# Kernel tuning notes

Hardware: AMD Instinct MI355X
Metric: run time of the kernel (lower is better)

The kernel has to match this reference:

```python
import jax, jax.numpy as jnp
import numpy as np
import math

B, S, D, H = 8, 1024, 512, 8
DH = D // H
SCALE_BASE = 512


def _xpos(x, downscale):
    # x: [B, H, S, DH]; xpos rotary with exponential scale (jamie-stirling RetNet impl)
    s = x.shape[-2]
    d = x.shape[-1]
    half = d // 2
    sv = (jnp.arange(0, d, 2, dtype=jnp.float32) + 0.4 * d) / (1.4 * d)      # [half]
    power = jnp.arange(s, dtype=jnp.float32) / SCALE_BASE
    scale = sv[None, :] ** power[:, None]                                     # [s, half]
    inv_freq = 1.0 / (10000.0 ** (jnp.arange(half, dtype=jnp.float32) / half))
    ang = jnp.arange(s, dtype=jnp.float32)[:, None] * inv_freq[None, :]       # [s, half]
    if downscale:
        scale = 1.0 / scale
    sin = jnp.repeat(jnp.sin(ang) * scale, 2, axis=-1)                        # [s, d]
    cos = jnp.repeat(jnp.cos(ang) * scale, 2, axis=-1)
    rot = jnp.stack((-x[..., 1::2], x[..., ::2]), axis=-1).reshape(x.shape)   # rotate_every_two
    return x * cos + rot * sin


def setup_inputs() -> dict:
    key = jax.random.key(0)
    ks = jax.random.split(key, 7)
    X = jax.random.normal(ks[0], (B, S, D), dtype=jnp.float32)
    # per-head projections stacked: torch init randn/hidden_size
    W_Q = jax.random.normal(ks[1], (H, D, DH), dtype=jnp.float32) / D
    W_K = jax.random.normal(ks[2], (H, D, DH), dtype=jnp.float32) / D
    W_V = jax.random.normal(ks[3], (H, D, DH), dtype=jnp.float32) / D
    W_G = jax.random.normal(ks[4], (D, D), dtype=jnp.float32) / D
    W_O = jax.random.normal(ks[5], (D, D), dtype=jnp.float32) / D
    gn_weight = jnp.ones((D,), dtype=jnp.float32)
    gn_bias = jnp.zeros((D,), dtype=jnp.float32)
    return {"X": X, "W_Q": W_Q, "W_K": W_K, "W_V": W_V, "W_G": W_G,
            "W_O": W_O, "gn_weight": gn_weight, "gn_bias": gn_bias}


def reference(X, W_Q, W_K, W_V, W_G, W_O, gn_weight, gn_bias):
    b, s, _ = X.shape
    # per-head decay gammas and symmetric (non-causal) decay matrix D
    gammas = 1.0 - jnp.exp(jnp.linspace(math.log(1.0 / 32), math.log(1.0 / 512), H)).astype(jnp.float32)
    n = jnp.arange(s)
    Dmat = gammas[:, None, None] ** jnp.abs(n[:, None] - n[None, :]).astype(jnp.float32)  # [H,s,s]
    Q = _xpos(jnp.einsum('bsd,hde->bhse', X, W_Q), False)
    K = _xpos(jnp.einsum('bsd,hde->bhse', X, W_K), True)
    V = jnp.einsum('bsd,hde->bhse', X, W_V)
    scores = jnp.einsum('bhse,bhte->bhst', Q, K)
    p = jax.nn.softmax(scores, axis=-1) * Dmat[None]          # decay-weighted softmax
    Y = jnp.einsum('bhst,bhte->bhse', p, V)                    # [b,H,s,DH]
    Y = jnp.moveaxis(Y, 1, 2).reshape(b, s, H * DH)            # concat heads -> [b,s,D]
    # GroupNorm(H groups) over flattened rows [b*s, D]
    Yg = Y.reshape(-1, H, DH)
    mu = Yg.mean(axis=-1, keepdims=True)
    var = Yg.var(axis=-1, keepdims=True)
    Yn = ((Yg - mu) * jax.lax.rsqrt(var + 1e-5)).reshape(-1, H * DH)
    Yn = (Yn * gn_weight + gn_bias).reshape(b, s, H * DH)
    G = X @ W_G
    swish = G * jax.nn.sigmoid(G)
    return (swish * Yn) @ W_O
```

## Files before the change

### kernel.cpp

```cpp
#include <hip/hip_runtime.h>
#include <math.h>

#define B_ 8
#define S_ 1024
#define D_ 512
#define H_ 8
#define DH_ 64
#define M_ (B_*S_)

typedef __attribute__((ext_vector_type(8))) short short8;
typedef __attribute__((ext_vector_type(4))) short s16x4;
typedef __attribute__((ext_vector_type(4))) float f32x4;

__device__ inline void tsplit(float x, short& hs, short& ls) {
  unsigned u = __float_as_uint(x);
  hs = (short)(u >> 16);
  float r = x - __uint_as_float(u & 0xFFFF0000u);
  ls = (short)(__float_as_uint(r) >> 16);
}
__device__ inline f32x4 mfma16(short8 a, short8 b, f32x4 c) {
  return __builtin_amdgcn_mfma_f32_16x16x32_bf16(a, b, c, 0, 0, 0);
}
__device__ inline void gload_lds16(const void* g, void* l) {
  __builtin_amdgcn_global_load_lds(
      (const __attribute__((address_space(1))) void*)g,
      (__attribute__((address_space(3))) void*)l, 16, 0, 0);
}

__global__ void xpos_table_kernel(float* __restrict__ tab) {
  int idx = blockIdx.x * 256 + threadIdx.x;
  int s = idx >> 5, i = idx & 31;
  float sv = (2.0f * (float)i + 0.4f * 64.0f) / (1.4f * 64.0f);
  float p = (float)s / 512.0f;
  float scale = powf(sv, p);
  float inv_freq = powf(10000.0f, -((float)i / 32.0f));
  float ang = (float)s * inv_freq;
  float sn = sinf(ang), cs = cosf(ang);
  tab[idx]          = cs * scale;
  tab[32768 + idx]  = sn * scale;
  tab[65536 + idx]  = cs / scale;
  tab[98304 + idx]  = sn / scale;
}

__global__ __launch_bounds__(256) void wprep_kernel(
    const float* __restrict__ Wq, const float* __restrict__ Wk,
    const float* __restrict__ Wv, const float* __restrict__ Wg,
    short* __restrict__ BTh, short* __restrict__ BTl, int gonly) {
  __shared__ float t[64][65];
  const int n0 = blockIdx.x * 64, k0 = blockIdx.y * 64;
  const int tid = threadIdx.x;
  const float* src;
  int ld;
  if (gonly) {
    src = Wg + (size_t)k0 * 512 + n0; ld = 512;
  } else {
    int w = n0 >> 9, nn = n0 & 511;
    if (w == 3) { src = Wg + (size_t)k0 * 512 + nn; ld = 512; }
    else {
      const float* W = (w == 0) ? Wq : ((w == 1) ? Wk : Wv);
      int h = nn >> 6;
      src = W + (size_t)h * D_ * DH_ + (size_t)k0 * 64; ld = 64;
    }
  }
#pragma unroll
  for (int i = 0; i < 4; ++i) {
    int idx = tid + i * 256;
    int kk = idx >> 4, nl4 = (idx & 15) * 4;
    float4 v = *(const float4*)(src + (size_t)kk * ld + nl4);
    t[kk][nl4] = v.x; t[kk][nl4 + 1] = v.y; t[kk][nl4 + 2] = v.z; t[kk][nl4 + 3] = v.w;
  }
  __syncthreads();
#pragma unroll
  for (int i = 0; i < 2; ++i) {
    int idx = tid + i * 256;
    int nl = idx >> 3, ck = idx & 7;
    short8 hh, ll;
#pragma unroll
    for (int j = 0; j < 8; ++j) {
      short h_, l_;
      tsplit(t[ck * 8 + j][nl], h_, l_);
      hh[j] = h_; ll[j] = l_;
    }
    size_t off = (size_t)(n0 + nl) * 512 + k0 + ck * 8;
    *(short8*)(BTh + off) = hh;
    *(short8*)(BTl + off) = ll;
  }
}

template<int AMODE, int NSUB>
__global__ __launch_bounds__(256) void gemm_mfma_kernel(
    const float* __restrict__ Af,
    const short* __restrict__ Ah, const short* __restrict__ Al,
    const short* __restrict__ BTh, const short* __restrict__ BTl,
    const float* __restrict__ tab,
    short* __restrict__ QhO, short* __restrict__ QlO,
    short* __restrict__ KhO, short* __restrict__ KlO,
    short* __restrict__ VhT, short* __restrict__ VlT,
    float* __restrict__ G, int fused) {
  constexpr int NT = NSUB * 32;
  constexpr int ASTR = (AMODE == 0) ? 40 : 32;
  __shared__ __align__(16) short AsH[128][ASTR];
  __shared__ __align__(16) short AsL[128][ASTR];
  __shared__ __align__(16) short BsH[NT][32];
  __shared__ __align__(16) short BsL[NT][32];
  const int m0 = blockIdx.x * 128, by = blockIdx.y, n0 = by * NT;
  const int tid = threadIdx.x, w = tid >> 6, lane = tid & 63;
  const int lx = lane & 15, quad = lane >> 4;
  const int wr = w >> 1, wc = w & 1;
  f32x4 acc[4][NSUB] = {};
  for (int k0 = 0; k0 < 512; k0 += 32) {
    if constexpr (AMODE == 0) {
      int r = tid >> 1, cb = (tid & 1) * 16;
      const float* ap = Af + (size_t)(m0 + r) * 512 + k0 + cb;
      short8 hh[2], ll[2];
#pragma unroll
      for (int j4 = 0; j4 < 4; ++j4) {
        float4 v = *(const float4*)(ap + j4 * 4);
        short h_, l_;
        tsplit(v.x, h_, l_); hh[j4 >> 1][(j4 & 1) * 4 + 0] = h_; ll[j4 >> 1][(j4 & 1) * 4 + 0] = l_;
        tsplit(v.y, h_, l_); hh[j4 >> 1][(j4 & 1) * 4 + 1] = h_; ll[j4 >> 1][(j4 & 1) * 4 + 1] = l_;
        tsplit(v.z, h_, l_); hh[j4 >> 1][(j4 & 1) * 4 + 2] = h_; ll[j4 >> 1][(j4 & 1) * 4 + 2] = l_;
        tsplit(v.w, h_, l_); hh[j4 >> 1][(j4 & 1) * 4 + 3] = h_; ll[j4 >> 1][(j4 & 1) * 4 + 3] = l_;
      }
      *(short8*)&AsH[r][cb]     = hh[0];
      *(short8*)&AsH[r][cb + 8] = hh[1];
      *(short8*)&AsL[r][cb]     = ll[0];
      *(short8*)&AsL[r][cb + 8] = ll[1];
    } else {
#pragma unroll
      for (int c = 0; c < 2; ++c) {
        int ch = w + c * 4;
        size_t goff = (size_t)(m0 + ch * 16 + (lane >> 2)) * 512 + k0 + (lane & 3) * 8;
        gload_lds16(Ah + goff, &AsH[ch * 16][0]);
        gload_lds16(Al + goff, &AsL[ch * 16][0]);
      }
    }
    {
      constexpr int NCH = NT / 16;
#pragma unroll
      for (int ch = 0; ch < NCH; ch += 4) {
        int c = w + ch;
        if (c < NCH) {
          size_t goff = (size_t)(n0 + c * 16 + (lane >> 2)) * 512 + k0 + (lane & 3) * 8;
          gload_lds16(BTh + goff, &BsH[c * 16][0]);
          gload_lds16(BTl + goff, &BsL[c * 16][0]);
        }
      }
    }
    __syncthreads();
    short8 fah[4], fal[4], fbh[NSUB], fbl[NSUB];
#pragma unroll
    for (int i = 0; i < 4; ++i) {
      fah[i] = *(const short8*)&AsH[wr * 64 + i * 16 + lx][quad * 8];
      fal[i] = *(const short8*)&AsL[wr * 64 + i * 16 + lx][quad * 8];
    }
#pragma unroll
    for (int i = 0; i < NSUB; ++i) {
      fbh[i] = *(const short8*)&BsH[wc * (NSUB * 16) + i * 16 + lx][quad * 8];
      fbl[i] = *(const short8*)&BsL[wc * (NSUB * 16) + i * 16 + lx][quad * 8];
    }
#pragma unroll
    for (int ms = 0; ms < 4; ++ms)
#pragma unroll
      for (int ns = 0; ns < NSUB; ++ns) {
        f32x4 a = acc[ms][ns];
        a = mfma16(fah[ms], fbh[ns], a);
        a = mfma16(fal[ms], fbh[ns], a);
        a = mfma16(fah[ms], fbl[ns], a);
        acc[ms][ns] = a;
      }
    __syncthreads();
  }
  if (fused) {
    const int w4 = by >> 2;
    const int ncb = (by & 3) * 128 + wc * 64;
    if (w4 < 2) {
      short* Ph = (w4 == 0) ? QhO : KhO;
      short* Pl = (w4 == 0) ? QlO : KlO;
      const float* ct = tab + (w4 ? 65536 : 0);
      const float* st = tab + (w4 ? 98304 : 32768);
#pragma unroll
      for (int ms = 0; ms < 4; ++ms) {
        const int m = m0 + wr * 64 + ms * 16 + quad * 4;
        const int b = m >> 10, sbase = m & 1023;
#pragma unroll
        for (int ns = 0; ns < 4; ++ns) {
          const int n = ncb + ns * 16 + lx;
          const int h = n >> 6, e = n & 63;
          const int i0 = e >> 1;
          const float sgn = (e & 1) ? 1.0f : -1.0f;
          short* ph = Ph + (((size_t)(b * 8 + h)) * 1024 + sbase) * 64 + e;
          short* pl = Pl + (((size_t)(b * 8 + h)) * 1024 + sbase) * 64 + e;
#pragma unroll
          for (int rg = 0; rg < 4; ++rg) {
            const int s = sbase + rg;
            float v = acc[ms][ns][rg];
            float vp = __shfl_xor(v, 1);
            float o = v * ct[s * 32 + i0] + sgn * vp * st[s * 32 + i0];
            short h_, l_;
            tsplit(o, h_, l_);
            ph[rg * 64] = h_;
            pl[rg * 64] = l_;
          }
        }
      }
    } else if (w4 == 2) {
#pragma unroll
      for (int ms = 0; ms < 4; ++ms) {
        const int m = m0 + wr * 64 + ms * 16 + quad * 4;
        const int b = m >> 10, s = m & 1023;
#pragma unroll
        for (int ns = 0; ns < 4; ++ns) {
          const int n = ncb + ns * 16 + lx;
          const int h = n >> 6, e = n & 63;
          s16x4 hh, ll;
#pragma unroll
          for (int rg = 0; rg < 4; ++rg) {
            short h_, l_;
            tsplit(acc[ms][ns][rg], h_, l_);
            hh[rg] = h_; ll[rg] = l_;
          }
          size_t off = (((size_t)(b * 8 + h)) * 64 + e) * 1024 + s;
          *(s16x4*)(VhT + off) = hh;
          *(s16x4*)(VlT + off) = ll;
        }
      }
    } else {
#pragma unroll
      for (int ms = 0; ms < 4; ++ms) {
        const int m = m0 + wr * 64 + ms * 16 + quad * 4;
#pragma unroll
        for (int ns = 0; ns < 4; ++ns) {
          const int n = ncb + ns * 16 + lx;
#pragma unroll
          for (int rg = 0; rg < 4; ++rg) G[(size_t)(m + rg) * 512 + n] = acc[ms][ns][rg];
        }
      }
    }
  } else {
#pragma unroll
    for (int ms = 0; ms < 4; ++ms) {
      const int m = m0 + wr * 64 + ms * 16 + quad * 4;
#pragma unroll
      for (int ns = 0; ns < NSUB; ++ns) {
        const int n = n0 + wc * (NSUB * 16) + ns * 16 + lx;
#pragma unroll
        for (int rg = 0; rg < 4; ++rg) G[(size_t)(m + rg) * 512 + n] = acc[ms][ns][rg];
      }
    }
  }
}

__global__ __launch_bounds__(256, 2) void attn_mfma_kernel(
    const short* __restrict__ Qh, const short* __restrict__ Ql,
    const short* __restrict__ Kh, const short* __restrict__ Kl,
    const short* __restrict__ VhT, const short* __restrict__ VlT,
    const float* __restrict__ Gp,
    const float* __restrict__ gnw, const float* __restrict__ gnb,
    short* __restrict__ Zh, short* __restrict__ Zl) {
  __shared__ __align__(16) short KhS[64][72];
  __shared__ __align__(16) short KlS[64][72];
  __shared__ __align__(16) short VhS[64][72];
  __shared__ __align__(16) short VlS[64][72];
  __shared__ __align__(16) short PhS[4][32][72];
  const int bh = blockIdx.x, s0 = blockIdx.y * 128;
  const int b = bh >> 3, h = bh & 7;
  const int tid = threadIdx.x;
  const int w = tid >> 6, lane = tid & 63;
  const int lx = lane & 15, quad = lane >> 4;
  const int s0w = s0 + w * 32;
  const float l0c = -3.4657359027997265f;
  const float l1c = -6.2383246250395075f;
  const float gamma = 1.0f - expf(l0c + (float)h * (l1c - l0c) / 7.0f);
  const float lg2g = log2f(gamma);
  const short* Qbh = Qh + (size_t)bh * S_ * DH_;
  const short* Qbl = Ql + (size_t)bh * S_ * DH_;
  const short* Kbh = Kh + (size_t)bh * S_ * DH_;
  const short* Kbl = Kl + (size_t)bh * S_ * DH_;
  const short* VbH = VhT + (size_t)bh * DH_ * S_;
  const short* VbL = VlT + (size_t)bh * DH_ * S_;

  float cl[4], cr[4], w4g[4], b4g[4];
#pragma unroll
  for (int ns = 0; ns < 4; ++ns) {
    cl[ns] = exp2f(lg2g * (float)(ns * 16 + lx));
    cr[ns] = exp2f(lg2g * (float)(63 - ns * 16 - lx));
    w4g[ns] = gnw[h * DH_ + ns * 16 + lx];
    b4g[ns] = gnb[h * DH_ + ns * 16 + lx];
  }

  short8 qfh[2][2], qfl[2][2];
#pragma unroll
  for (int ms = 0; ms < 2; ++ms)
#pragma unroll
    for (int kc = 0; kc < 2; ++kc) {
      size_t off = (size_t)(s0w + ms * 16 + lx) * DH_ + kc * 32 + quad * 8;
      qfh[ms][kc] = *(const short8*)(Qbh + off);
      qfl[ms][kc] = *(const short8*)(Qbl + off);
    }

  f32x4 O[2][4] = {};
  float lsum[2][4] = {};

  for (int t0 = 0; t0 < S_; t0 += 64) {
    __syncthreads();
#pragma unroll
    for (int i = 0; i < 2; ++i) {
      int slot = tid + i * 256;
      int r = slot >> 3, c8 = (slot & 7) * 8;
      *(short8*)&KhS[r][c8] = *(const short8*)(Kbh + (size_t)(t0 + r) * DH_ + c8);
      *(short8*)&KlS[r][c8] = *(const short8*)(Kbl + (size_t)(t0 + r) * DH_ + c8);
      *(short8*)&VhS[r][c8] = *(const short8*)(VbH + (size_t)r * S_ + t0 + c8);
      *(short8*)&VlS[r][c8] = *(const short8*)(VbL + (size_t)r * S_ + t0 + c8);
    }
    __syncthreads();
    f32x4 acc[2][4];
#pragma unroll
    for (int ns = 0; ns < 4; ++ns) {
      short8 kh0 = *(const short8*)&KhS[ns * 16 + lx][quad * 8];
      short8 kh1 = *(const short8*)&KhS[ns * 16 + lx][32 + quad * 8];
      short8 kl0 = *(const short8*)&KlS[ns * 16 + lx][quad * 8];
      short8 kl1 = *(const short8*)&KlS[ns * 16 + lx][32 + quad * 8];
#pragma unroll
      for (int ms = 0; ms < 2; ++ms) {
        f32x4 a = {};
        a = mfma16(qfh[ms][0], kh0, a);
        a = mfma16(qfl[ms][0], kh0, a);
        a = mfma16(qfh[ms][0], kl0, a);
        a = mfma16(qfh[ms][1], kh1, a);
        a = mfma16(qfl[ms][1], kh1, a);
        a = mfma16(qfh[ms][1], kl1, a);
        acc[ms][ns] = a;
      }
    }
    const int cse = (t0 + 63 < s0w) ? 0 : ((t0 > s0w + 31) ? 1 : 2);
#pragma unroll
    for (int ms = 0; ms < 2; ++ms)
#pragma unroll
      for (int rg = 0; rg < 4; ++rg) {
        const int rloc = ms * 16 + quad * 4 + rg;
        const int srow = s0w + rloc;
        float pe[4], p[4];
#pragma unroll
        for (int ns = 0; ns < 4; ++ns) pe[ns] = __expf(acc[ms][ns][rg]);
        lsum[ms][rg] += (pe[0] + pe[1]) + (pe[2] + pe[3]);
        if (cse == 0) {
          float rf = exp2f(lg2g * (float)(srow - t0 - 63));
#pragma unroll
          for (int ns = 0; ns < 4; ++ns) p[ns] = pe[ns] * rf * cr[ns];
        } else if (cse == 1) {
          float rf = exp2f(lg2g * (float)(t0 - srow));
#pragma unroll
          for (int ns = 0; ns < 4; ++ns) p[ns] = pe[ns] * rf * cl[ns];
        } else {
#pragma unroll
          for (int ns = 0; ns < 4; ++ns)
            p[ns] = pe[ns] * exp2f(lg2g * fabsf((float)(srow - (t0 + ns * 16 + lx))));
        }
#pragma unroll
        for (int ns = 0; ns < 4; ++ns)
          PhS[w][rloc][ns * 16 + lx] = (short)((__float_as_uint(p[ns]) + 0x8000u) >> 16);
      }
    short8 pf[2][2];
#pragma unroll
    for (int ms = 0; ms < 2; ++ms)
#pragma unroll
      for (int kc = 0; kc < 2; ++kc)
        pf[ms][kc] = *(const short8*)&PhS[w][ms * 16 + lx][kc * 32 + quad * 8];
#pragma unroll
    for (int ns = 0; ns < 4; ++ns) {
      short8 vh0 = *(const short8*)&VhS[ns * 16 + lx][quad * 8];
      short8 vh1 = *(const short8*)&VhS[ns * 16 + lx][32 + quad * 8];
      short8 vl0 = *(const short8*)&VlS[ns * 16 + lx][quad * 8];
      short8 vl1 = *(const short8*)&VlS[ns * 16 + lx][32 + quad * 8];
#pragma unroll
      for (int ms = 0; ms < 2; ++ms) {
        f32x4 o = O[ms][ns];
        o = mfma16(pf[ms][0], vh0, o);
        o = mfma16(pf[ms][0], vl0, o);
        o = mfma16(pf[ms][1], vh1, o);
        o = mfma16(pf[ms][1], vl1, o);
        O[ms][ns] = o;
      }
    }
  }
#pragma unroll
  for (int ms = 0; ms < 2; ++ms)
#pragma unroll
    for (int rg = 0; rg < 4; ++rg) {
      float s = lsum[ms][rg];
      s += __shfl_xor(s, 1);
      s += __shfl_xor(s, 2);
      s += __shfl_xor(s, 4);
      s += __shfl_xor(s, 8);
      const float inv = 1.0f / s;
      const int srow = s0w + ms * 16 + quad * 4 + rg;
      float y[4];
      float rs = 0.0f;
#pragma unroll
      for (int ns = 0; ns < 4; ++ns) { y[ns] = O[ms][ns][rg] * inv; rs += y[ns]; }
      rs += __shfl_xor(rs, 1);
      rs += __shfl_xor(rs, 2);
      rs += __shfl_xor(rs, 4);
      rs += __shfl_xor(rs, 8);
      const float mu = rs * (1.0f / 64.0f);
      float vv = 0.0f;
#pragma unroll
      for (int ns = 0; ns < 4; ++ns) { float d = y[ns] - mu; vv += d * d; }
      vv += __shfl_xor(vv, 1);
      vv += __shfl_xor(vv, 2);
      vv += __shfl_xor(vv, 4);
      vv += __shfl_xor(vv, 8);
      const float rstd = rsqrtf(vv * (1.0f / 64.0f) + 1e-5f);
      const size_t base = (size_t)(b * S_ + srow) * D_ + h * DH_;
#pragma unroll
      for (int ns = 0; ns < 4; ++ns) {
        float g = Gp[base + ns * 16 + lx];
        float sw = g / (1.0f + __expf(-g));
        float z = sw * ((y[ns] - mu) * rstd * w4g[ns] + b4g[ns]);
        short zh_, zl_;
        tsplit(z, zh_, zl_);
        Zh[base + ns * 16 + lx] = zh_;
        Zl[base + ns * 16 + lx] = zl_;
      }
    }
}

extern "C" void kernel_launch(void* const* d_in, const int* in_sizes, int n_in,
                              void* d_out, int out_size, void* d_ws, size_t ws_size,
                              hipStream_t stream) {
  const float* X   = (const float*)d_in[0];
  const float* Wq  = (const float*)d_in[1];
  const float* Wk  = (const float*)d_in[2];
  const float* Wv  = (const float*)d_in[3];
  const float* Wg  = (const float*)d_in[4];
  const float* Wo  = (const float*)d_in[5];
  const float* gnw = (const float*)d_in[6];
  const float* gnb = (const float*)d_in[7];
  float* out = (float*)d_out;
  float* ws  = (float*)d_ws;
  const size_t NB = (size_t)M_ * D_;
  float* R0 = ws;
  float* R1 = ws + NB;
  float* R2 = ws + 2 * NB;
  float* R3 = ws + 3 * NB;
  float* tab = ws + 4 * NB;
  short* BTh = (short*)R3;
  short* BTl = BTh + (size_t)2048 * 512;
  short* Qh = (short*)R0;  short* Ql = Qh + NB;
  short* Kh = (short*)R1;  short* Kl = Kh + NB;
  short* VhT = (short*)R2; short* VlT = VhT + NB;
  short* Zh = (short*)R3;  short* Zl = Zh + NB;
  short* BToh = (short*)R1;
  short* BTol = BToh + (size_t)512 * 512;

  wprep_kernel<<<dim3(32, 8), 256, 0, stream>>>(Wq, Wk, Wv, Wg, BTh, BTl, 0);
  xpos_table_kernel<<<128, 256, 0, stream>>>(tab);
  gemm_mfma_kernel<0, 4><<<dim3(64, 16), 256, 0, stream>>>(
      X, nullptr, nullptr, BTh, BTl, tab, Qh, Ql, Kh, Kl, VhT, VlT, out, 1);
  attn_mfma_kernel<<<dim3(64, 8), 256, 0, stream>>>(
      Qh, Ql, Kh, Kl, VhT, VlT, out, gnw, gnb, Zh, Zl);
  wprep_kernel<<<dim3(8, 8), 256, 0, stream>>>(nullptr, nullptr, nullptr, Wo, BToh, BTol, 1);
  gemm_mfma_kernel<1, 2><<<dim3(64, 8), 256, 0, stream>>>(
      nullptr, Zh, Zl, BToh, BTol, nullptr, nullptr, nullptr, nullptr, nullptr,
      nullptr, nullptr, out, 0);
}
```

Baseline: 227.8 us.

## Double-buffer GEMM LDS tiles with fragment-ordered operand layouts

Reworks both MFMA GEMMs into a double-buffered pipeline: the next k-tile is loaded straight into LDS while the current tile is computed, with one barrier pair per iteration. Weights and the Z intermediate are now stored pre-tiled in MFMA-fragment order, so global-to-LDS copies are contiguous and fragment reads are simple linear LDS loads. The fp32 X operand is staged raw, with an XOR swizzle to avoid bank conflicts, and split into bf16 hi/lo at fragment-load time. The aim is to hide global load latency and cut LDS conversion work, at the cost of doubled LDS footprint and hand-tuned waitcnt counts that must match the issued loads.

```diff
diff --git a/kernel.cpp b/kernel.cpp
--- a/kernel.cpp
+++ b/kernel.cpp
@@ -11,6 +11,7 @@
 typedef __attribute__((ext_vector_type(8))) short short8;
 typedef __attribute__((ext_vector_type(4))) short s16x4;
 typedef __attribute__((ext_vector_type(4))) float f32x4;
+typedef __attribute__((ext_vector_type(4))) unsigned int u32x4;
 
 __device__ inline void tsplit(float x, short& hs, short& ls) {
   unsigned u = __float_as_uint(x);
@@ -18,6 +19,25 @@
   float r = x - __uint_as_float(u & 0xFFFF0000u);
   ls = (short)(__float_as_uint(r) >> 16);
 }
+__device__ inline void splitpack(f32x4 a, f32x4 b, short8& hh, short8& ll) {
+  union { u32x4 u; short8 s; } H, L;
+#pragma unroll
+  for (int j = 0; j < 2; ++j) {
+    unsigned u0 = __float_as_uint(a[2 * j]);
+    unsigned u1 = __float_as_uint(a[2 * j + 1]);
+    H.u[j] = (u0 >> 16) | (u1 & 0xFFFF0000u);
+    float r0 = a[2 * j]     - __uint_as_float(u0 & 0xFFFF0000u);
+    float r1 = a[2 * j + 1] - __uint_as_float(u1 & 0xFFFF0000u);
+    L.u[j] = (__float_as_uint(r0) >> 16) | (__float_as_uint(r1) & 0xFFFF0000u);
+    unsigned v0 = __float_as_uint(b[2 * j]);
+    unsigned v1 = __float_as_uint(b[2 * j + 1]);
+    H.u[2 + j] = (v0 >> 16) | (v1 & 0xFFFF0000u);
+    float s0 = b[2 * j]     - __uint_as_float(v0 & 0xFFFF0000u);
+    float s1 = b[2 * j + 1] - __uint_as_float(v1 & 0xFFFF0000u);
+    L.u[2 + j] = (__float_as_uint(s0) >> 16) | (__float_as_uint(s1) & 0xFFFF0000u);
+  }
+  hh = H.s; ll = L.s;
+}
 __device__ inline f32x4 mfma16(short8 a, short8 b, f32x4 c) {
   return __builtin_amdgcn_mfma_f32_16x16x32_bf16(a, b, c, 0, 0, 0);
 }
@@ -26,6 +46,7 @@
       (const __attribute__((address_space(1))) void*)g,
       (__attribute__((address_space(3))) void*)l, 16, 0, 0);
 }
+
 
 __global__ void xpos_table_kernel(float* __restrict__ tab) {
   int idx = blockIdx.x * 256 + threadIdx.x;
@@ -81,14 +102,17 @@
       tsplit(t[ck * 8 + j][nl], h_, l_);
       hh[j] = h_; ll[j] = l_;
     }
-    size_t off = (size_t)(n0 + nl) * 512 + k0 + ck * 8;
+    const int n = n0 + nl, k = k0 + ck * 8;
+    const size_t off = ((size_t)((n >> 7) * 16 + (k >> 5))) * 4096
+                     + (size_t)((n >> 4) & 7) * 512
+                     + (size_t)(((k >> 3) & 3) * 16 + (n & 15)) * 8;
     *(short8*)(BTh + off) = hh;
     *(short8*)(BTl + off) = ll;
   }
 }
 
 template<int AMODE, int NSUB>
-__global__ __launch_bounds__(256) void gemm_mfma_kernel(
+__global__ __launch_bounds__(256, 2) void gemm_mfma_kernel(
     const float* __restrict__ Af,
     const short* __restrict__ Ah, const short* __restrict__ Al,
     const short* __restrict__ BTh, const short* __restrict__ BTl,
@@ -96,68 +120,94 @@
     short* __restrict__ QhO, short* __restrict__ QlO,
     short* __restrict__ KhO, short* __restrict__ KlO,
     short* __restrict__ VhT, short* __restrict__ VlT,
-    float* __restrict__ G, int fused) {
+    float* __restrict__ G) {
   constexpr int NT = NSUB * 32;
-  constexpr int ASTR = (AMODE == 0) ? 40 : 32;
-  __shared__ __align__(16) short AsH[128][ASTR];
-  __shared__ __align__(16) short AsL[128][ASTR];
-  __shared__ __align__(16) short BsH[NT][32];
-  __shared__ __align__(16) short BsL[NT][32];
-  const int m0 = blockIdx.x * 128, by = blockIdx.y, n0 = by * NT;
+  constexpr int BSZ = NT * 32;
+  constexpr int AFSZ = (AMODE == 0) ? 2 * 4096 : 4;
+  constexpr int ASSZ = (AMODE == 1) ? 2 * 4096 : 4;
+  __shared__ __align__(16) float AsF[AFSZ];
+  __shared__ __align__(16) short AsH[ASSZ], AsL[ASSZ];
+  __shared__ __align__(16) short BsH[2 * BSZ], BsL[2 * BSZ];
+  const int m0 = blockIdx.x * 128, by = blockIdx.y;
   const int tid = threadIdx.x, w = tid >> 6, lane = tid & 63;
   const int lx = lane & 15, quad = lane >> 4;
   const int wr = w >> 1, wc = w & 1;
   f32x4 acc[4][NSUB] = {};
-  for (int k0 = 0; k0 < 512; k0 += 32) {
+
+  auto stage = [&](int bsel, int kt) {
     if constexpr (AMODE == 0) {
-      int r = tid >> 1, cb = (tid & 1) * 16;
-      const float* ap = Af + (size_t)(m0 + r) * 512 + k0 + cb;
-      short8 hh[2], ll[2];
-#pragma unroll
-      for (int j4 = 0; j4 < 4; ++j4) {
-        float4 v = *(const float4*)(ap + j4 * 4);
-        short h_, l_;
-        tsplit(v.x, h_, l_); hh[j4 >> 1][(j4 & 1) * 4 + 0] = h_; ll[j4 >> 1][(j4 & 1) * 4 + 0] = l_;
-        tsplit(v.y, h_, l_); hh[j4 >> 1][(j4 & 1) * 4 + 1] = h_; ll[j4 >> 1][(j4 & 1) * 4 + 1] = l_;
-        tsplit(v.z, h_, l_); hh[j4 >> 1][(j4 & 1) * 4 + 2] = h_; ll[j4 >> 1][(j4 & 1) * 4 + 2] = l_;
-        tsplit(v.w, h_, l_); hh[j4 >> 1][(j4 & 1) * 4 + 3] = h_; ll[j4 >> 1][(j4 & 1) * 4 + 3] = l_;
-      }
-      *(short8*)&AsH[r][cb]     = hh[0];
-      *(short8*)&AsH[r][cb + 8] = hh[1];
-      *(short8*)&AsL[r][cb]     = ll[0];
-      *(short8*)&AsL[r][cb + 8] = ll[1];
+      const int r8 = lane >> 3, cg = (lane & 7) ^ r8;
+      const float* ab = Af + (size_t)(m0 + r8) * 512 + kt * 32 + cg * 4;
+      float* ad = &AsF[bsel * 4096];
+#pragma unroll
+      for (int c = 0; c < 4; ++c) {
+        const int ch = w * 4 + c;
+        gload_lds16(ab + (size_t)ch * (8 * 512), ad + ch * 256);
+      }
     } else {
-#pragma unroll
-      for (int c = 0; c < 2; ++c) {
-        int ch = w + c * 4;
-        size_t goff = (size_t)(m0 + ch * 16 + (lane >> 2)) * 512 + k0 + (lane & 3) * 8;
-        gload_lds16(Ah + goff, &AsH[ch * 16][0]);
-        gload_lds16(Al + goff, &AsL[ch * 16][0]);
-      }
-    }
-    {
-      constexpr int NCH = NT / 16;
-#pragma unroll
-      for (int ch = 0; ch < NCH; ch += 4) {
-        int c = w + ch;
-        if (c < NCH) {
-          size_t goff = (size_t)(n0 + c * 16 + (lane >> 2)) * 512 + k0 + (lane & 3) * 8;
-          gload_lds16(BTh + goff, &BsH[c * 16][0]);
-          gload_lds16(BTl + goff, &BsL[c * 16][0]);
-        }
-      }
-    }
-    __syncthreads();
+      const size_t ta = ((size_t)blockIdx.x * 16 + kt) * 4096 + lane * 8;
+      gload_lds16(Ah + ta + (size_t)w * 512,       &AsH[bsel * 4096 + w * 512]);
+      gload_lds16(Ah + ta + (size_t)(w + 4) * 512, &AsH[bsel * 4096 + (w + 4) * 512]);
+      gload_lds16(Al + ta + (size_t)w * 512,       &AsL[bsel * 4096 + w * 512]);
+      gload_lds16(Al + ta + (size_t)(w + 4) * 512, &AsL[bsel * 4096 + (w + 4) * 512]);
+    }
+    if constexpr (NSUB == 4) {
+      const size_t tb = ((size_t)by * 16 + kt) * 4096 + lane * 8;
+      gload_lds16(BTh + tb + (size_t)w * 512,       &BsH[bsel * BSZ + w * 512]);
+      gload_lds16(BTh + tb + (size_t)(w + 4) * 512, &BsH[bsel * BSZ + (w + 4) * 512]);
+      gload_lds16(BTl + tb + (size_t)w * 512,       &BsL[bsel * BSZ + w * 512]);
+      gload_lds16(BTl + tb + (size_t)(w + 4) * 512, &BsL[bsel * BSZ + (w + 4) * 512]);
+    } else {
+      const size_t tb = ((size_t)(by >> 1) * 16 + kt) * 4096
+                      + (size_t)(by & 1) * 2048 + lane * 8;
+      const short* src = (w < 2) ? BTh : BTl;
+      short* dst = (w < 2) ? &BsH[bsel * BSZ] : &BsL[bsel * BSZ];
+      const int wq = (w & 1) * 2;
+      gload_lds16(src + tb + (size_t)wq * 512,       dst + wq * 512);
+      gload_lds16(src + tb + (size_t)(wq + 1) * 512, dst + (wq + 1) * 512);
+    }
+  };
+
+  stage(0, 0);
+  int cur = 0;
+  for (int t = 0; t < 16; ++t) {
+    asm volatile("s_waitcnt lgkmcnt(0)" ::: "memory");
+    __builtin_amdgcn_s_barrier();
+    asm volatile("" ::: "memory");
+    if (t < 15) {
+      stage(cur ^ 1, t + 1);
+      if constexpr (AMODE == 0)
+        asm volatile("s_waitcnt vmcnt(8)" ::: "memory");
+      else
+        asm volatile("s_waitcnt vmcnt(6)" ::: "memory");
+    } else {
+      asm volatile("s_waitcnt vmcnt(0)" ::: "memory");
+    }
+    __builtin_amdgcn_s_barrier();
+    asm volatile("" ::: "memory");
+
     short8 fah[4], fal[4], fbh[NSUB], fbl[NSUB];
-#pragma unroll
-    for (int i = 0; i < 4; ++i) {
-      fah[i] = *(const short8*)&AsH[wr * 64 + i * 16 + lx][quad * 8];
-      fal[i] = *(const short8*)&AsL[wr * 64 + i * 16 + lx][quad * 8];
+    if constexpr (AMODE == 0) {
+      const float* ab = &AsF[cur * 4096];
+#pragma unroll
+      for (int i = 0; i < 4; ++i) {
+        const int row = wr * 64 + i * 16 + lx;
+        f32x4 x0 = *(const f32x4*)(ab + row * 32 + (((quad * 2)     ^ (lx & 7)) * 4));
+        f32x4 x1 = *(const f32x4*)(ab + row * 32 + (((quad * 2 + 1) ^ (lx & 7)) * 4));
+        splitpack(x0, x1, fah[i], fal[i]);
+      }
+    } else {
+#pragma unroll
+      for (int i = 0; i < 4; ++i) {
+        fah[i] = *(const short8*)&AsH[cur * 4096 + (wr * 4 + i) * 512 + lane * 8];
+        fal[i] = *(const short8*)&AsL[cur * 4096 + (wr * 4 + i) * 512 + lane * 8];
+      }
     }
 #pragma unroll
     for (int i = 0; i < NSUB; ++i) {
-      fbh[i] = *(const short8*)&BsH[wc * (NSUB * 16) + i * 16 + lx][quad * 8];
-      fbl[i] = *(const short8*)&BsL[wc * (NSUB * 16) + i * 16 + lx][quad * 8];
+      const int g = (NSUB == 4 ? wc * 4 : wc * 2) + i;
+      fbh[i] = *(const short8*)&BsH[cur * BSZ + g * 512 + lane * 8];
+      fbl[i] = *(const short8*)&BsL[cur * BSZ + g * 512 + lane * 8];
     }
 #pragma unroll
     for (int ms = 0; ms < 4; ++ms)
@@ -169,9 +219,9 @@
         a = mfma16(fah[ms], fbl[ns], a);
         acc[ms][ns] = a;
       }
-    __syncthreads();
-  }
-  if (fused) {
+    cur ^= 1;
+  }
+  if constexpr (AMODE == 0) {
     const int w4 = by >> 2;
     const int ncb = (by & 3) * 128 + wc * 64;
     if (w4 < 2) {
@@ -243,7 +293,7 @@
       const int m = m0 + wr * 64 + ms * 16 + quad * 4;
 #pragma unroll
       for (int ns = 0; ns < NSUB; ++ns) {
-        const int n = n0 + wc * (NSUB * 16) + ns * 16 + lx;
+        const int n = by * NT + wc * (NSUB * 16) + ns * 16 + lx;
 #pragma unroll
         for (int rg = 0; rg < 4; ++rg) G[(size_t)(m + rg) * 512 + n] = acc[ms][ns][rg];
       }
@@ -413,6 +463,9 @@
       vv += __shfl_xor(vv, 8);
       const float rstd = rsqrtf(vv * (1.0f / 64.0f) + 1e-5f);
       const size_t base = (size_t)(b * S_ + srow) * D_ + h * DH_;
+      const int m = b * S_ + srow;
+      const size_t zb = ((size_t)((m >> 7) * 16 + h * 2)) * 4096
+                      + (size_t)((m >> 4) & 7) * 512 + (size_t)(m & 15) * 8;
 #pragma unroll
       for (int ns = 0; ns < 4; ++ns) {
         float g = Gp[base + ns * 16 + lx];
@@ -420,8 +473,10 @@
         float z = sw * ((y[ns] - mu) * rstd * w4g[ns] + b4g[ns]);
         short zh_, zl_;
         tsplit(z, zh_, zl_);
-        Zh[base + ns * 16 + lx] = zh_;
-        Zl[base + ns * 16 + lx] = zl_;
+        const size_t off = zb + (size_t)(ns >> 1) * 4096
+                         + (size_t)(((ns * 2 + (lx >> 3)) & 3) * 128) + (lx & 7);
+        Zh[off] = zh_;
+        Zl[off] = zl_;
       }
     }
 }
@@ -457,11 +512,11 @@
   wprep_kernel<<<dim3(32, 8), 256, 0, stream>>>(Wq, Wk, Wv, Wg, BTh, BTl, 0);
   xpos_table_kernel<<<128, 256, 0, stream>>>(tab);
   gemm_mfma_kernel<0, 4><<<dim3(64, 16), 256, 0, stream>>>(
-      X, nullptr, nullptr, BTh, BTl, tab, Qh, Ql, Kh, Kl, VhT, VlT, out, 1);
+      X, nullptr, nullptr, BTh, BTl, tab, Qh, Ql, Kh, Kl, VhT, VlT, out);
   attn_mfma_kernel<<<dim3(64, 8), 256, 0, stream>>>(
       Qh, Ql, Kh, Kl, VhT, VlT, out, gnw, gnb, Zh, Zl);
   wprep_kernel<<<dim3(8, 8), 256, 0, stream>>>(nullptr, nullptr, nullptr, Wo, BToh, BTol, 1);
   gemm_mfma_kernel<1, 2><<<dim3(64, 8), 256, 0, stream>>>(
       nullptr, Zh, Zl, BToh, BTol, nullptr, nullptr, nullptr, nullptr, nullptr,
-      nullptr, nullptr, out, 0);
-}
+      nullptr, nullptr, out);
+}
```

Result: faster. 223.3 us (-2.0%).
